# Optimization experiments

Measured on AMD Instinct MI355X. Metric: run time of the kernel, lower is better.

The kernel has to match this reference:

```python
import jax, jax.numpy as jnp
import numpy as np

IN_FEATURES = 4096
OUT_FEATURES = 11008
BLOCK_SIZE = 256
BPR = IN_FEATURES // BLOCK_SIZE  # blocks per row = 16


def setup_inputs() -> dict:
    key = jax.random.key(0)
    k1, k2, k3, k4, k5 = jax.random.split(key, 5)
    x = jax.random.normal(k1, (2, 2048, IN_FEATURES), dtype=jnp.float32)
    indices = jax.random.randint(k2, (OUT_FEATURES, IN_FEATURES), 0, 256, dtype=jnp.int32)
    scales = jax.random.uniform(k3, (OUT_FEATURES * BPR,), dtype=jnp.float32)
    biases_ab = jax.random.normal(k4, (OUT_FEATURES * BPR,), dtype=jnp.float32) * 0.02
    bias = jax.random.normal(k5, (OUT_FEATURES,), dtype=jnp.float32)
    return {"x": x, "indices": indices, "scales": scales, "biases_ab": biases_ab, "bias": bias}


def _dequant(indices, scales, biases_ab):
    # W[i, j] = ((idx - 128) / 127) * scale[block] + bias_ab[block]
    q = (indices.astype(jnp.float32) - 128.0) / 127.0          # [O, I]
    q = q.reshape(OUT_FEATURES, BPR, BLOCK_SIZE)               # [O, bpr, bs]
    s = scales.reshape(OUT_FEATURES, BPR, 1)
    b = biases_ab.reshape(OUT_FEATURES, BPR, 1)
    return (q * s + b).reshape(OUT_FEATURES, IN_FEATURES)      # [O, I]


def reference(x, indices, scales, biases_ab, bias):
    W = _dequant(indices, scales, biases_ab)                   # [O, I]
    x2d = x.reshape(-1, IN_FEATURES)                           # [N, I]
    out = jnp.einsum('ni,oi->no', x2d, W) + bias[None, :]      # [N, O]
    return out.reshape(*x.shape[:-1], OUT_FEATURES)
```

## Files before the change

kernel.cpp:

```cpp
#include <hip/hip_runtime.h>

#define K_DIM 4096
#define O_DIM 11008
#define QBLK  256
#define BPR   (K_DIM / QBLK)

typedef _Float16 f16;
typedef _Float16 f16x8 __attribute__((ext_vector_type(8)));
typedef float    f32x4 __attribute__((ext_vector_type(4)));

__global__ __launch_bounds__(256) void cvt_x_kernel(const float* __restrict__ x,
                                                    f16* __restrict__ xh) {
    size_t i = ((size_t)blockIdx.x * 256 + threadIdx.x) * 8;
    float4 a = *(const float4*)(x + i);
    float4 b = *(const float4*)(x + i + 4);
    f16x8 h;
    h[0] = (f16)a.x; h[1] = (f16)a.y; h[2] = (f16)a.z; h[3] = (f16)a.w;
    h[4] = (f16)b.x; h[5] = (f16)b.y; h[6] = (f16)b.z; h[7] = (f16)b.w;
    *(f16x8*)(xh + i) = h;
}

__global__ __launch_bounds__(256) void dequant_w_kernel(const int* __restrict__ qidx,
                                                        const float* __restrict__ scales,
                                                        const float* __restrict__ babs,
                                                        f16* __restrict__ wh) {
    size_t e = ((size_t)blockIdx.x * 256 + threadIdx.x) * 8;
    int4 q0 = *(const int4*)(qidx + e);
    int4 q1 = *(const int4*)(qidx + e + 4);
    int sb = (int)(e >> 8);
    float s2 = scales[sb] * (1.0f / 127.0f);
    float b2 = fmaf(-128.0f, s2, babs[sb]);
    f16x8 h;
    h[0] = (f16)fmaf((float)q0.x, s2, b2);
    h[1] = (f16)fmaf((float)q0.y, s2, b2);
    h[2] = (f16)fmaf((float)q0.z, s2, b2);
    h[3] = (f16)fmaf((float)q0.w, s2, b2);
    h[4] = (f16)fmaf((float)q1.x, s2, b2);
    h[5] = (f16)fmaf((float)q1.y, s2, b2);
    h[6] = (f16)fmaf((float)q1.z, s2, b2);
    h[7] = (f16)fmaf((float)q1.w, s2, b2);
    *(f16x8*)(wh + e) = h;
}

#define BM 256
#define BN 256
#define BK 32
#define NT (K_DIM / BK)
#define NBN (O_DIM / BN)
#define TILE_E (BM * BK)

__global__ __launch_bounds__(512, 2) void gemm256_f16_kernel(const f16* __restrict__ A,
                                                             const f16* __restrict__ B,
                                                             const float* __restrict__ bias,
                                                             float* __restrict__ out) {
    __shared__ f16 smem[4][2][TILE_E];

    int bid = blockIdx.x;
    int chunk = gridDim.x >> 3;
    int swz = (bid & 7) * chunk + (bid >> 3);
    int bm = swz / NBN;
    int bn = swz - bm * NBN;

    const int tid  = threadIdx.x;
    const int lane = tid & 63;
    const int wid  = tid >> 6;
    const int wr   = wid >> 2;
    const int wc   = wid & 3;
    const int fr   = lane & 15;
    const int fq   = lane >> 4;

    const f16* gA = A + (size_t)bm * BM * K_DIM;
    const f16* gB = B + (size_t)bn * BN * K_DIM;

    const int srow  = tid >> 2;
    const int sslot = (tid & 3) ^ ((tid >> 3) & 3);
    const size_t goff = (size_t)srow * K_DIM + sslot * 8;
    const int loff = tid * 8;

    int aoffs[8], boffs[4];
    #pragma unroll
    for (int m = 0; m < 8; ++m) {
        int r = wr * 128 + m * 16 + fr;
        aoffs[m] = r * BK + ((fq ^ ((r >> 1) & 3)) << 3);
    }
    #pragma unroll
    for (int n = 0; n < 4; ++n) {
        int r = wc * 64 + n * 16 + fr;
        boffs[n] = r * BK + ((fq ^ ((r >> 1) & 3)) << 3);
    }

    f32x4 acc[8][4];
    #pragma unroll
    for (int m = 0; m < 8; ++m)
        #pragma unroll
        for (int n = 0; n < 4; ++n)
            acc[m][n] = (f32x4){0.f, 0.f, 0.f, 0.f};

#define STAGE(tt)                                                                        \
    do {                                                                                 \
        int _b = (tt) & 3;                                                               \
        size_t _k = (size_t)(tt) * BK;                                                   \
        __builtin_amdgcn_global_load_lds(                                                \
            (const __attribute__((address_space(1))) void*)(gA + _k + goff),             \
            (__attribute__((address_space(3))) void*)(&smem[_b][0][loff]), 16, 0, 0);    \
        __builtin_amdgcn_global_load_lds(                                                \
            (const __attribute__((address_space(1))) void*)(gA + _k + goff + (size_t)128 * K_DIM), \
            (__attribute__((address_space(3))) void*)(&smem[_b][0][loff + 4096]), 16, 0, 0); \
        __builtin_amdgcn_global_load_lds(                                                \
            (const __attribute__((address_space(1))) void*)(gB + _k + goff),             \
            (__attribute__((address_space(3))) void*)(&smem[_b][1][loff]), 16, 0, 0);    \
        __builtin_amdgcn_global_load_lds(                                                \
            (const __attribute__((address_space(1))) void*)(gB + _k + goff + (size_t)128 * K_DIM), \
            (__attribute__((address_space(3))) void*)(&smem[_b][1][loff + 4096]), 16, 0, 0); \
    } while (0)

    STAGE(0);
    STAGE(1);
    STAGE(2);

    for (int t = 0; t < NT; ++t) {
        __builtin_amdgcn_s_barrier();

        if (t < NT - 3) {
            STAGE(t + 3);
            asm volatile("s_waitcnt vmcnt(12)" ::: "memory");
        } else if (t == NT - 3) {
            asm volatile("s_waitcnt vmcnt(8)" ::: "memory");
        } else if (t == NT - 2) {
            asm volatile("s_waitcnt vmcnt(4)" ::: "memory");
        } else {
            asm volatile("s_waitcnt vmcnt(0)" ::: "memory");
        }

        __builtin_amdgcn_s_barrier();

        const f16* Asb = &smem[t & 3][0][0];
        const f16* Bsb = &smem[t & 3][1][0];

        f16x8 af[8], bf[4];
        #pragma unroll
        for (int m = 0; m < 8; ++m)
            af[m] = *(const f16x8*)(Asb + aoffs[m]);
        #pragma unroll
        for (int n = 0; n < 4; ++n)
            bf[n] = *(const f16x8*)(Bsb + boffs[n]);

        __builtin_amdgcn_s_setprio(1);
        #pragma unroll
        for (int m = 0; m < 8; ++m)
            #pragma unroll
            for (int n = 0; n < 4; ++n)
                acc[m][n] = __builtin_amdgcn_mfma_f32_16x16x32_f16(af[m], bf[n], acc[m][n], 0, 0, 0);
        __builtin_amdgcn_s_setprio(0);
    }
#undef STAGE

    #pragma unroll
    for (int m = 0; m < 8; ++m) {
        int grow = bm * BM + wr * 128 + m * 16 + fq * 4;
        #pragma unroll
        for (int n = 0; n < 4; ++n) {
            int gcol = bn * BN + wc * 64 + n * 16 + fr;
            float bv = bias[gcol];
            #pragma unroll
            for (int r = 0; r < 4; ++r)
                out[(size_t)(grow + r) * O_DIM + gcol] = acc[m][n][r] + bv;
        }
    }
}

__global__ __launch_bounds__(256) void fallback_kernel(const float* __restrict__ x,
                                                       const int* __restrict__ qidx,
                                                       const float* __restrict__ scales,
                                                       const float* __restrict__ babs,
                                                       const float* __restrict__ bias,
                                                       float* __restrict__ out) {
    __shared__ float xs[K_DIM];
    int n = blockIdx.x;
    int o = blockIdx.y * 256 + threadIdx.x;
    for (int i = threadIdx.x; i < K_DIM; i += 256)
        xs[i] = x[(size_t)n * K_DIM + i];
    __syncthreads();
    const int* qr = qidx + (size_t)o * K_DIM;
    float sum = 0.f;
    for (int b = 0; b < BPR; ++b) {
        float s2 = scales[o * BPR + b] * (1.0f / 127.0f);
        float b2 = fmaf(-128.0f, s2, babs[o * BPR + b]);
        for (int k = 0; k < QBLK; ++k)
            sum = fmaf(xs[b * QBLK + k], fmaf((float)qr[b * QBLK + k], s2, b2), sum);
    }
    out[(size_t)n * O_DIM + o] = sum + bias[o];
}

extern "C" void kernel_launch(void* const* d_in, const int* in_sizes, int n_in,
                              void* d_out, int out_size, void* d_ws, size_t ws_size,
                              hipStream_t stream) {
    const float* x      = (const float*)d_in[0];
    const int*   qidx   = (const int*)d_in[1];
    const float* scales = (const float*)d_in[2];
    const float* babs   = (const float*)d_in[3];
    const float* bias   = (const float*)d_in[4];
    float* out = (float*)d_out;

    const int nrows = in_sizes[0] / K_DIM;

    const size_t xh_bytes = (size_t)nrows * K_DIM * sizeof(f16);
    const size_t wh_bytes = (size_t)O_DIM * K_DIM * sizeof(f16);

    if (ws_size >= xh_bytes + wh_bytes && (nrows % BM) == 0) {
        f16* xh = (f16*)d_ws;
        f16* wh = (f16*)((char*)d_ws + xh_bytes);

        int cvt_blocks = (int)(((size_t)nrows * K_DIM) / 2048);
        cvt_x_kernel<<<cvt_blocks, 256, 0, stream>>>(x, xh);

        int dq_blocks = (int)(((size_t)O_DIM * K_DIM) / 2048);
        dequant_w_kernel<<<dq_blocks, 256, 0, stream>>>(qidx, scales, babs, wh);

        int nwg = (nrows / BM) * NBN;
        gemm256_f16_kernel<<<nwg, 512, 0, stream>>>(xh, wh, bias, out);
    } else {
        dim3 grid(nrows, O_DIM / 256);
        fallback_kernel<<<grid, 256, 0, stream>>>(x, qidx, scales, babs, bias, out);
    }
}
```

Measured before the change: 727.2 us.

## Restructure GEMM main loop into 8-phase pipeline with BK=64 double buffering

Measured after the change: 702.9 us. 1.03x faster.

```diff
diff --git a/kernel.cpp b/kernel.cpp
--- a/kernel.cpp
+++ b/kernel.cpp
@@ -44,16 +44,15 @@
 
 #define BM 256
 #define BN 256
-#define BK 32
+#define BK 64
 #define NT (K_DIM / BK)
 #define NBN (O_DIM / BN)
-#define TILE_E (BM * BK)
-
-__global__ __launch_bounds__(512, 2) void gemm256_f16_kernel(const f16* __restrict__ A,
-                                                             const f16* __restrict__ B,
-                                                             const float* __restrict__ bias,
-                                                             float* __restrict__ out) {
-    __shared__ f16 smem[4][2][TILE_E];
+
+__global__ __launch_bounds__(512, 2) void gemm8p_f16_kernel(const f16* __restrict__ A,
+                                                            const f16* __restrict__ B,
+                                                            const float* __restrict__ bias,
+                                                            float* __restrict__ out) {
+    __shared__ f16 sm[2][4][8192];
 
     int bid = blockIdx.x;
     int chunk = gridDim.x >> 3;
@@ -74,19 +73,21 @@
 
     const int srow  = tid >> 2;
     const int sslot = (tid & 3) ^ ((tid >> 3) & 3);
-    const size_t goff = (size_t)srow * K_DIM + sslot * 8;
-    const int loff = tid * 8;
-
-    int aoffs[8], boffs[4];
-    #pragma unroll
-    for (int m = 0; m < 8; ++m) {
-        int r = wr * 128 + m * 16 + fr;
-        aoffs[m] = r * BK + ((fq ^ ((r >> 1) & 3)) << 3);
-    }
+    const size_t gsoff = (size_t)srow * K_DIM + sslot * 8;
+    const int ldst = tid * 8;
+
+    int offa[2][4], offb[4];
+    #pragma unroll
+    for (int mh = 0; mh < 2; ++mh)
+        #pragma unroll
+        for (int ml = 0; ml < 4; ++ml) {
+            int r = wr * 128 + mh * 64 + ml * 16 + fr;
+            offa[mh][ml] = r * 32 + ((fq ^ ((r >> 1) & 3)) << 3);
+        }
     #pragma unroll
     for (int n = 0; n < 4; ++n) {
         int r = wc * 64 + n * 16 + fr;
-        boffs[n] = r * BK + ((fq ^ ((r >> 1) & 3)) << 3);
+        offb[n] = r * 32 + ((fq ^ ((r >> 1) & 3)) << 3);
     }
 
     f32x4 acc[8][4];
@@ -96,68 +97,96 @@
         for (int n = 0; n < 4; ++n)
             acc[m][n] = (f32x4){0.f, 0.f, 0.f, 0.f};
 
-#define STAGE(tt)                                                                        \
-    do {                                                                                 \
-        int _b = (tt) & 3;                                                               \
-        size_t _k = (size_t)(tt) * BK;                                                   \
-        __builtin_amdgcn_global_load_lds(                                                \
-            (const __attribute__((address_space(1))) void*)(gA + _k + goff),             \
-            (__attribute__((address_space(3))) void*)(&smem[_b][0][loff]), 16, 0, 0);    \
-        __builtin_amdgcn_global_load_lds(                                                \
-            (const __attribute__((address_space(1))) void*)(gA + _k + goff + (size_t)128 * K_DIM), \
-            (__attribute__((address_space(3))) void*)(&smem[_b][0][loff + 4096]), 16, 0, 0); \
-        __builtin_amdgcn_global_load_lds(                                                \
-            (const __attribute__((address_space(1))) void*)(gB + _k + goff),             \
-            (__attribute__((address_space(3))) void*)(&smem[_b][1][loff]), 16, 0, 0);    \
-        __builtin_amdgcn_global_load_lds(                                                \
-            (const __attribute__((address_space(1))) void*)(gB + _k + goff + (size_t)128 * K_DIM), \
-            (__attribute__((address_space(3))) void*)(&smem[_b][1][loff + 4096]), 16, 0, 0); \
-    } while (0)
-
-    STAGE(0);
-    STAGE(1);
-    STAGE(2);
-
-    for (int t = 0; t < NT; ++t) {
-        __builtin_amdgcn_s_barrier();
-
-        if (t < NT - 3) {
-            STAGE(t + 3);
-            asm volatile("s_waitcnt vmcnt(12)" ::: "memory");
-        } else if (t == NT - 3) {
-            asm volatile("s_waitcnt vmcnt(8)" ::: "memory");
-        } else if (t == NT - 2) {
-            asm volatile("s_waitcnt vmcnt(4)" ::: "memory");
-        } else {
-            asm volatile("s_waitcnt vmcnt(0)" ::: "memory");
-        }
-
-        __builtin_amdgcn_s_barrier();
-
-        const f16* Asb = &smem[t & 3][0][0];
-        const f16* Bsb = &smem[t & 3][1][0];
-
-        f16x8 af[8], bf[4];
-        #pragma unroll
-        for (int m = 0; m < 8; ++m)
-            af[m] = *(const f16x8*)(Asb + aoffs[m]);
-        #pragma unroll
-        for (int n = 0; n < 4; ++n)
-            bf[n] = *(const f16x8*)(Bsb + boffs[n]);
-
-        __builtin_amdgcn_s_setprio(1);
-        #pragma unroll
-        for (int m = 0; m < 8; ++m)
-            #pragma unroll
-            for (int n = 0; n < 4; ++n)
-                acc[m][n] = __builtin_amdgcn_mfma_f32_16x16x32_f16(af[m], bf[n], acc[m][n], 0, 0, 0);
-        __builtin_amdgcn_s_setprio(0);
-    }
-#undef STAGE
+#define STAGE_HALF(T_, h_)                                                                   \
+    do {                                                                                     \
+        const f16* gsrc_ = ((h_) < 2) ? gA : gB;                                             \
+        size_t koff_ = (size_t)(T_) * BK + ((h_) & 1) * 32;                                  \
+        __builtin_amdgcn_global_load_lds(                                                    \
+            (const __attribute__((address_space(1))) void*)(gsrc_ + gsoff + koff_),          \
+            (__attribute__((address_space(3))) void*)(&sm[(T_) & 1][h_][ldst]), 16, 0, 0);   \
+        __builtin_amdgcn_global_load_lds(                                                    \
+            (const __attribute__((address_space(1))) void*)(gsrc_ + gsoff + koff_ + (size_t)128 * K_DIM), \
+            (__attribute__((address_space(3))) void*)(&sm[(T_) & 1][h_][ldst + 4096]), 16, 0, 0); \
+    } while (0)
+
+#define LOAD_AF(d_, kk_, mh_)                                                    \
+    do {                                                                         \
+        const f16* hb_ = &sm[d_][kk_][0];                                        \
+        af[0] = *(const f16x8*)(hb_ + offa[mh_][0]);                             \
+        af[1] = *(const f16x8*)(hb_ + offa[mh_][1]);                             \
+        af[2] = *(const f16x8*)(hb_ + offa[mh_][2]);                             \
+        af[3] = *(const f16x8*)(hb_ + offa[mh_][3]);                             \
+    } while (0)
+
+#define LOAD_BF(d_, kk_)                                                         \
+    do {                                                                         \
+        const f16* hb_ = &sm[d_][2 + (kk_)][0];                                  \
+        bf[0] = *(const f16x8*)(hb_ + offb[0]);                                  \
+        bf[1] = *(const f16x8*)(hb_ + offb[1]);                                  \
+        bf[2] = *(const f16x8*)(hb_ + offb[2]);                                  \
+        bf[3] = *(const f16x8*)(hb_ + offb[3]);                                  \
+    } while (0)
+
+#define MFMA16(mh_)                                                              \
+    do {                                                                         \
+        __builtin_amdgcn_s_setprio(1);                                           \
+        _Pragma("unroll")                                                        \
+        for (int ml = 0; ml < 4; ++ml)                                           \
+            _Pragma("unroll")                                                    \
+            for (int n = 0; n < 4; ++n)                                          \
+                acc[(mh_) * 4 + ml][n] =                                         \
+                    __builtin_amdgcn_mfma_f32_16x16x32_f16(af[ml], bf[n],        \
+                                                           acc[(mh_) * 4 + ml][n], 0, 0, 0); \
+        __builtin_amdgcn_s_setprio(0);                                           \
+    } while (0)
+
+    STAGE_HALF(0, 2); STAGE_HALF(0, 0); STAGE_HALF(0, 3); STAGE_HALF(0, 1);
+    STAGE_HALF(1, 2); STAGE_HALF(1, 0); STAGE_HALF(1, 3);
+    asm volatile("s_waitcnt vmcnt(10)" ::: "memory");
+    __builtin_amdgcn_s_barrier();
+
+    for (int T = 0; T < NT; ++T) {
+        const int d = T & 1;
+        f16x8 af[4], bf[4];
+
+        LOAD_AF(d, 0, 0);
+        LOAD_BF(d, 0);
+        if (T + 1 < NT) STAGE_HALF(T + 1, 1);
+        __builtin_amdgcn_s_barrier();
+        MFMA16(0);
+        __builtin_amdgcn_s_barrier();
+
+        LOAD_AF(d, 0, 1);
+        if (T + 2 < NT) STAGE_HALF(T + 2, 2);
+        if (T < NT - 2) asm volatile("s_waitcnt vmcnt(10)" ::: "memory");
+        else            asm volatile("s_waitcnt vmcnt(0)" ::: "memory");
+        __builtin_amdgcn_s_barrier();
+        MFMA16(1);
+        __builtin_amdgcn_s_barrier();
+
+        LOAD_AF(d, 1, 0);
+        LOAD_BF(d, 1);
+        if (T + 2 < NT) STAGE_HALF(T + 2, 0);
+        __builtin_amdgcn_s_barrier();
+        MFMA16(0);
+        __builtin_amdgcn_s_barrier();
+
+        LOAD_AF(d, 1, 1);
+        if (T + 2 < NT) STAGE_HALF(T + 2, 3);
+        if (T < NT - 2) asm volatile("s_waitcnt vmcnt(10)" ::: "memory");
+        else            asm volatile("s_waitcnt vmcnt(0)" ::: "memory");
+        __builtin_amdgcn_s_barrier();
+        MFMA16(1);
+        __builtin_amdgcn_s_barrier();
+    }
+#undef STAGE_HALF
+#undef LOAD_AF
+#undef LOAD_BF
+#undef MFMA16
 
     #pragma unroll
     for (int m = 0; m < 8; ++m) {
-        int grow = bm * BM + wr * 128 + m * 16 + fq * 4;
+        int grow = bm * BM + wr * 128 + (m >> 2) * 64 + (m & 3) * 16 + fq * 4;
         #pragma unroll
         for (int n = 0; n < 4; ++n) {
             int gcol = bn * BN + wc * 64 + n * 16 + fr;
@@ -218,7 +247,7 @@
         dequant_w_kernel<<<dq_blocks, 256, 0, stream>>>(qidx, scales, babs, wh);
 
         int nwg = (nrows / BM) * NBN;
-        gemm256_f16_kernel<<<nwg, 512, 0, stream>>>(xh, wh, bias, out);
+        gemm8p_f16_kernel<<<nwg, 512, 0, stream>>>(xh, wh, bias, out);
     } else {
         dim3 grid(nrows, O_DIM / 256);
         fallback_kernel<<<grid, 256, 0, stream>>>(x, qidx, scales, babs, bias, out);
```
